# Kernel tuning notes

Hardware: AMD Instinct MI355X
Metric: run time of the kernel (lower is better)

Reference implementation:

```python
import jax, jax.numpy as jnp
import numpy as np

NUM_HEADS = 8
DIM = 256  # == out_dim; module implicitly requires dim == out_dim


def setup_inputs() -> dict:
    key = jax.random.key(0)
    k0, k1, k2, k3, k4, k5 = jax.random.split(key, 6)
    B, N, T, dim = 4, 128, 128, DIM
    s = dim ** -0.5
    return {
        "v": jax.random.normal(k0, (B, N, T, dim), dtype=jnp.float32),
        "Wq": jax.random.normal(k1, (dim, dim), dtype=jnp.float32) * s,
        "Wk": jax.random.normal(k2, (dim, dim), dtype=jnp.float32) * s,
        "Wv": jax.random.normal(k3, (dim, dim), dtype=jnp.float32) * s,
        "Wp": jax.random.normal(k4, (dim, dim), dtype=jnp.float32) * s,
        "bp": jax.random.normal(k5, (dim,), dtype=jnp.float32) * 0.01,
    }


def reference(v, Wq, Wk, Wv, Wp, bp):
    B, N, T, dim = v.shape
    H = NUM_HEADS
    hd = dim // H
    scale = hd ** -0.5
    # projections (qkv_bias=False)
    q = (v @ Wq).reshape(B * N, T, H, hd)
    k = (v @ Wk).reshape(B * N, T, H, hd)
    vv = (v @ Wv).reshape(B * N, T, H, hd)
    # NOTE: heads axis is NOT moved before the matmul in the original torch
    # code, so attention is over the HEADS axis: per (b*n, t) an HxH matrix.
    attn = jnp.einsum('mthd,mtgd->mthg', q, k) * scale  # [B*N, T, H, H]
    attn = jax.nn.softmax(attn, axis=-1)
    x = jnp.einsum('mthg,mtgd->mthd', attn, vv).reshape(B, N, T, dim)
    # output projection (with bias); dropout probs are 0 / eval mode
    return x @ Wp + bp
```

## Files before the change

kernel.cpp:

```cpp
#include <hip/hip_runtime.h>
#include <hip/hip_bf16.h>
#include <math.h>


#define DIMX      256
#define NH        8
#define HD        32
#define TM        32
#define NTHREADS  512
#define ASTRIDE   264
#define QSTRIDE   776
#define NT_QKV    48
#define KT        8
#define NJ1       6
#define NJ2       2

typedef __bf16 bf16x8 __attribute__((ext_vector_type(8)));
typedef __bf16 bf16x4 __attribute__((ext_vector_type(4)));
typedef float  f32x4  __attribute__((ext_vector_type(4)));

__global__ void pack_weights(const float* __restrict__ Wq,
                             const float* __restrict__ Wk,
                             const float* __restrict__ Wv,
                             const float* __restrict__ Wp,
                             __bf16* __restrict__ pk)
{
    const int QKV_FRAGS = NT_QKV * KT * 64;
    int u = blockIdx.x * blockDim.x + threadIdx.x;
    const float* W;
    int nt, kt, lane;
    if (u < QKV_FRAGS) {
        nt = u / (KT * 64); kt = (u / 64) % KT; lane = u % 64;
        if (nt < 16)      { W = Wq; }
        else if (nt < 32) { W = Wk; nt -= 16; }
        else              { W = Wv; nt -= 32; }
    } else {
        int u2 = u - QKV_FRAGS;
        nt = u2 / (KT * 64); kt = (u2 / 64) % KT; lane = u2 % 64;
        W = Wp;
    }
    const int n  = nt * 16 + (lane & 15);
    const int k0 = kt * 32 + (lane >> 4) * 8;
    bf16x8 frag;
#pragma unroll
    for (int j = 0; j < 8; ++j)
        frag[j] = (__bf16)W[(size_t)(k0 + j) * DIMX + n];
    *(bf16x8*)(pk + (size_t)u * 8) = frag;
}

__global__ __launch_bounds__(NTHREADS, 4)
void fused_attn_mfma(const float* __restrict__ v,
                     const __bf16* __restrict__ Wqkv_pk,
                     const __bf16* __restrict__ Wp_pk,
                     const float* __restrict__ bp,
                     float* __restrict__ out)
{
    __shared__ __align__(16) unsigned short smem[TM * ASTRIDE + TM * QSTRIDE];
    unsigned short* As  = smem;
    unsigned short* QKV = smem + TM * ASTRIDE;

    const int tid   = threadIdx.x;
    const int lane  = tid & 63;
    const int wv_id = tid >> 6;
    const int l15   = lane & 15;
    const int quad  = lane >> 4;
    const long token0 = (long)blockIdx.x * TM;

    {
        const float4* src = (const float4*)(v + token0 * DIMX);
#pragma unroll
        for (int i = 0; i < 4; ++i) {
            int u = tid + NTHREADS * i;
            int m = u >> 6;
            int c = (u & 63) * 4;
            float4 t4 = src[u];
            bf16x4 b4 = { (__bf16)t4.x, (__bf16)t4.y, (__bf16)t4.z, (__bf16)t4.w };
            *(bf16x4*)&As[m * ASTRIDE + c] = b4;
        }
    }
    __syncthreads();

    {
        const int nt0 = wv_id * NJ1;
        f32x4 acc[2][NJ1];
#pragma unroll
        for (int tt = 0; tt < 2; ++tt)
#pragma unroll
            for (int j = 0; j < NJ1; ++j)
                acc[tt][j] = (f32x4){0.f, 0.f, 0.f, 0.f};

        const bf16x8* wb = (const bf16x8*)Wqkv_pk + lane;
        bf16x8 wcur[NJ1];
#pragma unroll
        for (int j = 0; j < NJ1; ++j)
            wcur[j] = wb[(size_t)((nt0 + j) * KT) * 64];

        for (int kt = 0; kt < KT; ++kt) {
            const int ktn = (kt + 1 < KT) ? kt + 1 : KT - 1;
            bf16x8 wnxt[NJ1];
#pragma unroll
            for (int j = 0; j < NJ1; ++j)
                wnxt[j] = wb[(size_t)((nt0 + j) * KT + ktn) * 64];

            bf16x8 vf[2];
#pragma unroll
            for (int tt = 0; tt < 2; ++tt)
                vf[tt] = *(const bf16x8*)&As[(tt * 16 + l15) * ASTRIDE + kt * 32 + quad * 8];

#pragma unroll
            for (int j = 0; j < NJ1; ++j) {
                acc[0][j] = __builtin_amdgcn_mfma_f32_16x16x32_bf16(wcur[j], vf[0], acc[0][j], 0, 0, 0);
                acc[1][j] = __builtin_amdgcn_mfma_f32_16x16x32_bf16(wcur[j], vf[1], acc[1][j], 0, 0, 0);
            }
#pragma unroll
            for (int j = 0; j < NJ1; ++j) wcur[j] = wnxt[j];
        }
#pragma unroll
        for (int tt = 0; tt < 2; ++tt)
#pragma unroll
            for (int j = 0; j < NJ1; ++j) {
                bf16x4 p4 = { (__bf16)acc[tt][j][0], (__bf16)acc[tt][j][1],
                              (__bf16)acc[tt][j][2], (__bf16)acc[tt][j][3] };
                *(bf16x4*)&QKV[(tt * 16 + l15) * QSTRIDE + (nt0 + j) * 16 + quad * 4] = p4;
            }
    }
    __syncthreads();

    {
        const int ta  = tid >> 4;
        const int sub = tid & 15;
        const int h   = sub >> 1;
        const int d0  = (sub & 1) * 16;
        const float scale = 0.17677669529663687f;

        const unsigned short* qrow  = &QKV[ta * QSTRIDE + h * HD + d0];
        const unsigned short* kbase = &QKV[ta * QSTRIDE + 256 + d0];
        const unsigned short* vbase = &QKV[ta * QSTRIDE + 512 + d0];

        float q[16];
#pragma unroll
        for (int s = 0; s < 2; ++s) {
            bf16x8 t = *(const bf16x8*)(qrow + s * 8);
#pragma unroll
            for (int j = 0; j < 8; ++j) q[s * 8 + j] = (float)t[j];
        }
        float logits[NH];
#pragma unroll
        for (int g = 0; g < NH; ++g) {
            float s = 0.f;
#pragma unroll
            for (int sg = 0; sg < 2; ++sg) {
                bf16x8 t = *(const bf16x8*)(kbase + g * HD + sg * 8);
#pragma unroll
                for (int j = 0; j < 8; ++j) s += q[sg * 8 + j] * (float)t[j];
            }
            logits[g] = s;
        }
#pragma unroll
        for (int g = 0; g < NH; ++g)
            logits[g] = (logits[g] + __shfl_xor(logits[g], 1, 64)) * scale;

        float mx = logits[0];
#pragma unroll
        for (int g = 1; g < NH; ++g) mx = fmaxf(mx, logits[g]);
        float se = 0.f;
#pragma unroll
        for (int g = 0; g < NH; ++g) { logits[g] = __expf(logits[g] - mx); se += logits[g]; }
        float inv = 1.f / se;
#pragma unroll
        for (int g = 0; g < NH; ++g) logits[g] *= inv;

        float x[16];
#pragma unroll
        for (int d = 0; d < 16; ++d) x[d] = 0.f;
#pragma unroll
        for (int g = 0; g < NH; ++g) {
            float p = logits[g];
#pragma unroll
            for (int sg = 0; sg < 2; ++sg) {
                bf16x8 t = *(const bf16x8*)(vbase + g * HD + sg * 8);
#pragma unroll
                for (int j = 0; j < 8; ++j) x[sg * 8 + j] += p * (float)t[j];
            }
        }
        __syncthreads();
#pragma unroll
        for (int s = 0; s < 2; ++s) {
            bf16x8 o;
#pragma unroll
            for (int j = 0; j < 8; ++j) o[j] = (__bf16)x[s * 8 + j];
            *(bf16x8*)&As[ta * ASTRIDE + h * HD + d0 + s * 8] = o;
        }
    }
    __syncthreads();

    {
        const int nt0 = wv_id * NJ2;
        f32x4 acc[2][NJ2];
#pragma unroll
        for (int tt = 0; tt < 2; ++tt)
#pragma unroll
            for (int j = 0; j < NJ2; ++j)
                acc[tt][j] = (f32x4){0.f, 0.f, 0.f, 0.f};

        const bf16x8* wb = (const bf16x8*)Wp_pk + lane;
        bf16x8 wcur[NJ2];
#pragma unroll
        for (int j = 0; j < NJ2; ++j)
            wcur[j] = wb[(size_t)((nt0 + j) * KT) * 64];

        for (int kt = 0; kt < KT; ++kt) {
            const int ktn = (kt + 1 < KT) ? kt + 1 : KT - 1;
            bf16x8 wnxt[NJ2];
#pragma unroll
            for (int j = 0; j < NJ2; ++j)
                wnxt[j] = wb[(size_t)((nt0 + j) * KT + ktn) * 64];

            bf16x8 xf[2];
#pragma unroll
            for (int tt = 0; tt < 2; ++tt)
                xf[tt] = *(const bf16x8*)&As[(tt * 16 + l15) * ASTRIDE + kt * 32 + quad * 8];

#pragma unroll
            for (int j = 0; j < NJ2; ++j) {
                acc[0][j] = __builtin_amdgcn_mfma_f32_16x16x32_bf16(wcur[j], xf[0], acc[0][j], 0, 0, 0);
                acc[1][j] = __builtin_amdgcn_mfma_f32_16x16x32_bf16(wcur[j], xf[1], acc[1][j], 0, 0, 0);
            }
#pragma unroll
            for (int j = 0; j < NJ2; ++j) wcur[j] = wnxt[j];
        }
#pragma unroll
        for (int j = 0; j < NJ2; ++j) {
            f32x4 b = *(const f32x4*)&bp[(nt0 + j) * 16 + quad * 4];
#pragma unroll
            for (int tt = 0; tt < 2; ++tt) {
                f32x4 o = acc[tt][j] + b;
                *(f32x4*)&out[(token0 + tt * 16 + l15) * DIMX + (nt0 + j) * 16 + quad * 4] = o;
            }
        }
    }
}

extern "C" void kernel_launch(void* const* d_in, const int* in_sizes, int n_in,
                              void* d_out, int out_size, void* d_ws, size_t ws_size,
                              hipStream_t stream) {
    const float* v  = (const float*)d_in[0];
    const float* Wq = (const float*)d_in[1];
    const float* Wk = (const float*)d_in[2];
    const float* Wv = (const float*)d_in[3];
    const float* Wp = (const float*)d_in[4];
    const float* bp = (const float*)d_in[5];
    float* out = (float*)d_out;

    __bf16* pk = (__bf16*)d_ws;
    const __bf16* Wqkv_pk = pk;
    const __bf16* Wp_pk   = pk + (size_t)24576 * 8;

    pack_weights<<<256, 128, 0, stream>>>(Wq, Wk, Wv, Wp, pk);

    const int ntokens = in_sizes[0] / DIMX;
    fused_attn_mfma<<<ntokens / TM, NTHREADS, 0, stream>>>(v, Wqkv_pk, Wp_pk, bp, out);
}
```

Before: 163.9 us.

## Alias input and QKV buffers in shared memory, switch to fp16 packed math

Result: faster. 158.7 us (-3.2%).

```diff
diff --git a/kernel.cpp b/kernel.cpp
--- a/kernel.cpp
+++ b/kernel.cpp
@@ -8,22 +8,24 @@
 #define HD        32
 #define TM        32
 #define NTHREADS  512
-#define ASTRIDE   264
 #define QSTRIDE   776
+#define KT        8
 #define NT_QKV    48
-#define KT        8
-#define NJ1       6
-#define NJ2       2
-
-typedef __bf16 bf16x8 __attribute__((ext_vector_type(8)));
-typedef __bf16 bf16x4 __attribute__((ext_vector_type(4)));
-typedef float  f32x4  __attribute__((ext_vector_type(4)));
+
+typedef _Float16 f16x8 __attribute__((ext_vector_type(8)));
+typedef _Float16 f16x4 __attribute__((ext_vector_type(4)));
+typedef _Float16 f16x2 __attribute__((ext_vector_type(2)));
+typedef float    f32x4 __attribute__((ext_vector_type(4)));
+
+static __device__ __forceinline__ f16x2 pkrtz(float a, float b) {
+    return (f16x2)__builtin_amdgcn_cvt_pkrtz(a, b);
+}
 
 __global__ void pack_weights(const float* __restrict__ Wq,
                              const float* __restrict__ Wk,
                              const float* __restrict__ Wv,
                              const float* __restrict__ Wp,
-                             __bf16* __restrict__ pk)
+                             _Float16* __restrict__ pk)
 {
     const int QKV_FRAGS = NT_QKV * KT * 64;
     int u = blockIdx.x * blockDim.x + threadIdx.x;
@@ -41,23 +43,21 @@
     }
     const int n  = nt * 16 + (lane & 15);
     const int k0 = kt * 32 + (lane >> 4) * 8;
-    bf16x8 frag;
+    f16x8 frag;
 #pragma unroll
     for (int j = 0; j < 8; ++j)
-        frag[j] = (__bf16)W[(size_t)(k0 + j) * DIMX + n];
-    *(bf16x8*)(pk + (size_t)u * 8) = frag;
-}
-
-__global__ __launch_bounds__(NTHREADS, 4)
+        frag[j] = (_Float16)W[(size_t)(k0 + j) * DIMX + n];
+    *(f16x8*)(pk + (size_t)u * 8) = frag;
+}
+
+__global__ __launch_bounds__(NTHREADS, 6)
 void fused_attn_mfma(const float* __restrict__ v,
-                     const __bf16* __restrict__ Wqkv_pk,
-                     const __bf16* __restrict__ Wp_pk,
+                     const _Float16* __restrict__ Wqkv_pk,
+                     const _Float16* __restrict__ Wp_pk,
                      const float* __restrict__ bp,
                      float* __restrict__ out)
 {
-    __shared__ __align__(16) unsigned short smem[TM * ASTRIDE + TM * QSTRIDE];
-    unsigned short* As  = smem;
-    unsigned short* QKV = smem + TM * ASTRIDE;
+    __shared__ __align__(16) _Float16 S[TM * QSTRIDE];
 
     const int tid   = threadIdx.x;
     const int lane  = tid & 63;
@@ -74,56 +74,101 @@
             int m = u >> 6;
             int c = (u & 63) * 4;
             float4 t4 = src[u];
-            bf16x4 b4 = { (__bf16)t4.x, (__bf16)t4.y, (__bf16)t4.z, (__bf16)t4.w };
-            *(bf16x4*)&As[m * ASTRIDE + c] = b4;
-        }
-    }
-    __syncthreads();
-
-    {
-        const int nt0 = wv_id * NJ1;
-        f32x4 acc[2][NJ1];
-#pragma unroll
-        for (int tt = 0; tt < 2; ++tt)
-#pragma unroll
-            for (int j = 0; j < NJ1; ++j)
-                acc[tt][j] = (f32x4){0.f, 0.f, 0.f, 0.f};
-
-        const bf16x8* wb = (const bf16x8*)Wqkv_pk + lane;
-        bf16x8 wcur[NJ1];
-#pragma unroll
-        for (int j = 0; j < NJ1; ++j)
-            wcur[j] = wb[(size_t)((nt0 + j) * KT) * 64];
-
-        for (int kt = 0; kt < KT; ++kt) {
-            const int ktn = (kt + 1 < KT) ? kt + 1 : KT - 1;
-            bf16x8 wnxt[NJ1];
-#pragma unroll
-            for (int j = 0; j < NJ1; ++j)
-                wnxt[j] = wb[(size_t)((nt0 + j) * KT + ktn) * 64];
-
-            bf16x8 vf[2];
-#pragma unroll
-            for (int tt = 0; tt < 2; ++tt)
-                vf[tt] = *(const bf16x8*)&As[(tt * 16 + l15) * ASTRIDE + kt * 32 + quad * 8];
-
-#pragma unroll
-            for (int j = 0; j < NJ1; ++j) {
-                acc[0][j] = __builtin_amdgcn_mfma_f32_16x16x32_bf16(wcur[j], vf[0], acc[0][j], 0, 0, 0);
-                acc[1][j] = __builtin_amdgcn_mfma_f32_16x16x32_bf16(wcur[j], vf[1], acc[1][j], 0, 0, 0);
-            }
-#pragma unroll
-            for (int j = 0; j < NJ1; ++j) wcur[j] = wnxt[j];
-        }
-#pragma unroll
-        for (int tt = 0; tt < 2; ++tt)
-#pragma unroll
-            for (int j = 0; j < NJ1; ++j) {
-                bf16x4 p4 = { (__bf16)acc[tt][j][0], (__bf16)acc[tt][j][1],
-                              (__bf16)acc[tt][j][2], (__bf16)acc[tt][j][3] };
-                *(bf16x4*)&QKV[(tt * 16 + l15) * QSTRIDE + (nt0 + j) * 16 + quad * 4] = p4;
-            }
-    }
+            f16x2 lo = pkrtz(t4.x, t4.y), hi = pkrtz(t4.z, t4.w);
+            f16x4 b4 = { lo.x, lo.y, hi.x, hi.y };
+            *(f16x4*)&S[m * QSTRIDE + c] = b4;
+        }
+    }
+    __syncthreads();
+
+    f32x4 acc1[2][3];
+    int tiles1[3] = { 2 * wv_id, 2 * wv_id + 1, 40 + wv_id };
+    {
+        int tiles0[3] = { 16 + wv_id * 3, 17 + wv_id * 3, 18 + wv_id * 3 };
+
+        f32x4 acc0[2][3];
+#pragma unroll
+        for (int tt = 0; tt < 2; ++tt)
+#pragma unroll
+            for (int j = 0; j < 3; ++j)
+                acc0[tt][j] = (f32x4){0.f, 0.f, 0.f, 0.f};
+        {
+            const f16x8* wb = (const f16x8*)Wqkv_pk + lane;
+            f16x8 wcur[3];
+#pragma unroll
+            for (int j = 0; j < 3; ++j)
+                wcur[j] = wb[(size_t)(tiles0[j] * KT) * 64];
+            for (int kt = 0; kt < KT; ++kt) {
+                const int ktn = (kt + 1 < KT) ? kt + 1 : KT - 1;
+                f16x8 wnxt[3];
+#pragma unroll
+                for (int j = 0; j < 3; ++j)
+                    wnxt[j] = wb[(size_t)(tiles0[j] * KT + ktn) * 64];
+                f16x8 vf[2];
+#pragma unroll
+                for (int tt = 0; tt < 2; ++tt)
+                    vf[tt] = *(const f16x8*)&S[(tt * 16 + l15) * QSTRIDE + kt * 32 + quad * 8];
+#pragma unroll
+                for (int j = 0; j < 3; ++j) {
+                    acc0[0][j] = __builtin_amdgcn_mfma_f32_16x16x32_f16(wcur[j], vf[0], acc0[0][j], 0, 0, 0);
+                    acc0[1][j] = __builtin_amdgcn_mfma_f32_16x16x32_f16(wcur[j], vf[1], acc0[1][j], 0, 0, 0);
+                }
+#pragma unroll
+                for (int j = 0; j < 3; ++j) wcur[j] = wnxt[j];
+            }
+        }
+#pragma unroll
+        for (int tt = 0; tt < 2; ++tt)
+#pragma unroll
+            for (int j = 0; j < 3; ++j) {
+                f16x2 a = pkrtz(acc0[tt][j][0], acc0[tt][j][1]);
+                f16x2 b = pkrtz(acc0[tt][j][2], acc0[tt][j][3]);
+                f16x4 p4 = { a.x, a.y, b.x, b.y };
+                *(f16x4*)&S[(tt * 16 + l15) * QSTRIDE + tiles0[j] * 16 + quad * 4] = p4;
+            }
+
+#pragma unroll
+        for (int tt = 0; tt < 2; ++tt)
+#pragma unroll
+            for (int j = 0; j < 3; ++j)
+                acc1[tt][j] = (f32x4){0.f, 0.f, 0.f, 0.f};
+        {
+            const f16x8* wb = (const f16x8*)Wqkv_pk + lane;
+            f16x8 wcur[3];
+#pragma unroll
+            for (int j = 0; j < 3; ++j)
+                wcur[j] = wb[(size_t)(tiles1[j] * KT) * 64];
+            for (int kt = 0; kt < KT; ++kt) {
+                const int ktn = (kt + 1 < KT) ? kt + 1 : KT - 1;
+                f16x8 wnxt[3];
+#pragma unroll
+                for (int j = 0; j < 3; ++j)
+                    wnxt[j] = wb[(size_t)(tiles1[j] * KT + ktn) * 64];
+                f16x8 vf[2];
+#pragma unroll
+                for (int tt = 0; tt < 2; ++tt)
+                    vf[tt] = *(const f16x8*)&S[(tt * 16 + l15) * QSTRIDE + kt * 32 + quad * 8];
+#pragma unroll
+                for (int j = 0; j < 3; ++j) {
+                    acc1[0][j] = __builtin_amdgcn_mfma_f32_16x16x32_f16(wcur[j], vf[0], acc1[0][j], 0, 0, 0);
+                    acc1[1][j] = __builtin_amdgcn_mfma_f32_16x16x32_f16(wcur[j], vf[1], acc1[1][j], 0, 0, 0);
+                }
+#pragma unroll
+                for (int j = 0; j < 3; ++j) wcur[j] = wnxt[j];
+            }
+        }
+    }
+    __syncthreads();
+
+#pragma unroll
+    for (int tt = 0; tt < 2; ++tt)
+#pragma unroll
+        for (int j = 0; j < 3; ++j) {
+            f16x2 a = pkrtz(acc1[tt][j][0], acc1[tt][j][1]);
+            f16x2 b = pkrtz(acc1[tt][j][2], acc1[tt][j][3]);
+            f16x4 p4 = { a.x, a.y, b.x, b.y };
+            *(f16x4*)&S[(tt * 16 + l15) * QSTRIDE + tiles1[j] * 16 + quad * 4] = p4;
+        }
     __syncthreads();
 
     {
@@ -133,28 +178,25 @@
         const int d0  = (sub & 1) * 16;
         const float scale = 0.17677669529663687f;
 
-        const unsigned short* qrow  = &QKV[ta * QSTRIDE + h * HD + d0];
-        const unsigned short* kbase = &QKV[ta * QSTRIDE + 256 + d0];
-        const unsigned short* vbase = &QKV[ta * QSTRIDE + 512 + d0];
-
-        float q[16];
-#pragma unroll
-        for (int s = 0; s < 2; ++s) {
-            bf16x8 t = *(const bf16x8*)(qrow + s * 8);
-#pragma unroll
-            for (int j = 0; j < 8; ++j) q[s * 8 + j] = (float)t[j];
-        }
+        const _Float16* qrow  = &S[ta * QSTRIDE + h * HD + d0];
+        const _Float16* kbase = &S[ta * QSTRIDE + 256 + d0];
+        const _Float16* vbase = &S[ta * QSTRIDE + 512 + d0];
+
+        f16x8 q0 = *(const f16x8*)qrow;
+        f16x8 q1 = *(const f16x8*)(qrow + 8);
+
         float logits[NH];
 #pragma unroll
         for (int g = 0; g < NH; ++g) {
-            float s = 0.f;
-#pragma unroll
-            for (int sg = 0; sg < 2; ++sg) {
-                bf16x8 t = *(const bf16x8*)(kbase + g * HD + sg * 8);
-#pragma unroll
-                for (int j = 0; j < 8; ++j) s += q[sg * 8 + j] * (float)t[j];
-            }
-            logits[g] = s;
+            f16x8 k0 = *(const f16x8*)(kbase + g * HD);
+            f16x8 k1 = *(const f16x8*)(kbase + g * HD + 8);
+            f16x8 p  = q0 * k0;
+            p += q1 * k1;
+            f16x4 r4 = __builtin_shufflevector(p, p, 0, 1, 2, 3)
+                     + __builtin_shufflevector(p, p, 4, 5, 6, 7);
+            f16x2 r2 = __builtin_shufflevector(r4, r4, 0, 1)
+                     + __builtin_shufflevector(r4, r4, 2, 3);
+            logits[g] = (float)r2.x + (float)r2.y;
         }
 #pragma unroll
         for (int g = 0; g < NH; ++g)
@@ -167,70 +209,59 @@
 #pragma unroll
         for (int g = 0; g < NH; ++g) { logits[g] = __expf(logits[g] - mx); se += logits[g]; }
         float inv = 1.f / se;
-#pragma unroll
-        for (int g = 0; g < NH; ++g) logits[g] *= inv;
-
-        float x[16];
-#pragma unroll
-        for (int d = 0; d < 16; ++d) x[d] = 0.f;
+
+        f16x8 xa0 = (f16x8)(_Float16)0.f;
+        f16x8 xa1 = (f16x8)(_Float16)0.f;
 #pragma unroll
         for (int g = 0; g < NH; ++g) {
-            float p = logits[g];
-#pragma unroll
-            for (int sg = 0; sg < 2; ++sg) {
-                bf16x8 t = *(const bf16x8*)(vbase + g * HD + sg * 8);
-#pragma unroll
-                for (int j = 0; j < 8; ++j) x[sg * 8 + j] += p * (float)t[j];
-            }
+            _Float16 ph = (_Float16)(logits[g] * inv);
+            f16x8 pw = { ph, ph, ph, ph, ph, ph, ph, ph };
+            f16x8 v0 = *(const f16x8*)(vbase + g * HD);
+            f16x8 v1 = *(const f16x8*)(vbase + g * HD + 8);
+            xa0 += pw * v0;
+            xa1 += pw * v1;
         }
         __syncthreads();
-#pragma unroll
-        for (int s = 0; s < 2; ++s) {
-            bf16x8 o;
-#pragma unroll
-            for (int j = 0; j < 8; ++j) o[j] = (__bf16)x[s * 8 + j];
-            *(bf16x8*)&As[ta * ASTRIDE + h * HD + d0 + s * 8] = o;
-        }
-    }
-    __syncthreads();
-
-    {
-        const int nt0 = wv_id * NJ2;
-        f32x4 acc[2][NJ2];
-#pragma unroll
-        for (int tt = 0; tt < 2; ++tt)
-#pragma unroll
-            for (int j = 0; j < NJ2; ++j)
+        *(f16x8*)&S[ta * QSTRIDE + h * HD + d0]     = xa0;
+        *(f16x8*)&S[ta * QSTRIDE + h * HD + d0 + 8] = xa1;
+    }
+    __syncthreads();
+
+    {
+        const int nt0 = wv_id * 2;
+        f32x4 acc[2][2];
+#pragma unroll
+        for (int tt = 0; tt < 2; ++tt)
+#pragma unroll
+            for (int j = 0; j < 2; ++j)
                 acc[tt][j] = (f32x4){0.f, 0.f, 0.f, 0.f};
 
-        const bf16x8* wb = (const bf16x8*)Wp_pk + lane;
-        bf16x8 wcur[NJ2];
-#pragma unroll
-        for (int j = 0; j < NJ2; ++j)
+        const f16x8* wb = (const f16x8*)Wp_pk + lane;
+        f16x8 wcur[2];
+#pragma unroll
+        for (int j = 0; j < 2; ++j)
             wcur[j] = wb[(size_t)((nt0 + j) * KT) * 64];
 
         for (int kt = 0; kt < KT; ++kt) {
             const int ktn = (kt + 1 < KT) ? kt + 1 : KT - 1;
-            bf16x8 wnxt[NJ2];
-#pragma unroll
-            for (int j = 0; j < NJ2; ++j)
+            f16x8 wnxt[2];
+#pragma unroll
+            for (int j = 0; j < 2; ++j)
                 wnxt[j] = wb[(size_t)((nt0 + j) * KT + ktn) * 64];
-
-            bf16x8 xf[2];
+            f16x8 xf[2];
 #pragma unroll
             for (int tt = 0; tt < 2; ++tt)
-                xf[tt] = *(const bf16x8*)&As[(tt * 16 + l15) * ASTRIDE + kt * 32 + quad * 8];
-
-#pragma unroll
-            for (int j = 0; j < NJ2; ++j) {
-                acc[0][j] = __builtin_amdgcn_mfma_f32_16x16x32_bf16(wcur[j], xf[0], acc[0][j], 0, 0, 0);
-                acc[1][j] = __builtin_amdgcn_mfma_f32_16x16x32_bf16(wcur[j], xf[1], acc[1][j], 0, 0, 0);
-            }
-#pragma unroll
-            for (int j = 0; j < NJ2; ++j) wcur[j] = wnxt[j];
-        }
-#pragma unroll
-        for (int j = 0; j < NJ2; ++j) {
+                xf[tt] = *(const f16x8*)&S[(tt * 16 + l15) * QSTRIDE + kt * 32 + quad * 8];
+#pragma unroll
+            for (int j = 0; j < 2; ++j) {
+                acc[0][j] = __builtin_amdgcn_mfma_f32_16x16x32_f16(wcur[j], xf[0], acc[0][j], 0, 0, 0);
+                acc[1][j] = __builtin_amdgcn_mfma_f32_16x16x32_f16(wcur[j], xf[1], acc[1][j], 0, 0, 0);
+            }
+#pragma unroll
+            for (int j = 0; j < 2; ++j) wcur[j] = wnxt[j];
+        }
+#pragma unroll
+        for (int j = 0; j < 2; ++j) {
             f32x4 b = *(const f32x4*)&bp[(nt0 + j) * 16 + quad * 4];
 #pragma unroll
             for (int tt = 0; tt < 2; ++tt) {
@@ -252,9 +283,9 @@
     const float* bp = (const float*)d_in[5];
     float* out = (float*)d_out;
 
-    __bf16* pk = (__bf16*)d_ws;
-    const __bf16* Wqkv_pk = pk;
-    const __bf16* Wp_pk   = pk + (size_t)24576 * 8;
+    _Float16* pk = (_Float16*)d_ws;
+    const _Float16* Wqkv_pk = pk;
+    const _Float16* Wp_pk   = pk + (size_t)24576 * 8;
 
     pack_weights<<<256, 128, 0, stream>>>(Wq, Wk, Wv, Wp, pk);
 
```
